# Performance work log

Hardware: AMD Instinct MI355X
Metric: run time of the kernel (lower is better)

## Reference

```python
import jax, jax.numpy as jnp
import numpy as np

D_IN, D_K, D_V = 512, 256, 256
B, S = 8, 2048

def _glorot(key, shape):
    fan_in, fan_out = shape[0], shape[-1]
    lim = np.sqrt(6.0 / (fan_in + fan_out))
    return jax.random.uniform(key, shape, jnp.float32, -lim, lim)

def setup_inputs() -> dict:
    key = jax.random.key(0)
    ks = jax.random.split(key, 9)
    return {
        "q_in": jax.random.normal(ks[0], (B, S, D_IN), jnp.float32),
        "k_in": jax.random.normal(ks[1], (B, S, D_IN), jnp.float32),
        "v_in": jax.random.normal(ks[2], (B, S, D_IN), jnp.float32),
        "Wq": _glorot(ks[3], (D_IN, D_K)),
        "bq": _glorot(ks[4], (1, D_K))[0],
        "Wk": _glorot(ks[5], (D_IN, D_K)),
        "bk": _glorot(ks[6], (1, D_K))[0],
        "Wv": _glorot(ks[7], (D_IN, D_V)),
        "bv": _glorot(ks[8], (1, D_V))[0],
    }

def reference(q_in, k_in, v_in, Wq, bq, Wk, bk, Wv, bv):
    # Dense projections (with bias, glorot-init'ed bias as in the original)
    q = q_in @ Wq + bq            # [B, S, d_k]
    k = k_in @ Wk + bk            # [B, S, d_k]
    v = v_in @ Wv + bv            # [B, S, d_v]
    scale = 1.0 / np.sqrt(D_K).astype(np.float32)
    # full attention matrix, scaled (map_fn in original == elementwise divide)
    attn = jnp.einsum('bqd,bkd->bqk', q, k) * scale  # [B, S, S]
    attn = jax.nn.softmax(attn, axis=-1)
    return jnp.einsum('bqk,bkd->bqd', attn, v)       # [B, S, d_v]
```

## Files before the change

kernel.cpp:

```cpp
#include <hip/hip_runtime.h>
#include <hip/hip_bf16.h>


typedef __attribute__((ext_vector_type(4))) float f32x4;
typedef __attribute__((ext_vector_type(8))) short s16x8;
typedef __attribute__((ext_vector_type(4))) short s16x4;

static __device__ __forceinline__ short f2bf(float x) {
  __hip_bfloat16 h = __float2bfloat16(x);
  return *reinterpret_cast<short*>(&h);
}
static __device__ __forceinline__ unsigned pack2bf(float lo, float hi) {
  return (unsigned)(unsigned short)f2bf(lo) |
         ((unsigned)(unsigned short)f2bf(hi) << 16);
}

__global__ __launch_bounds__(256) void proj3(
    const float* __restrict__ q_in, const float* __restrict__ k_in,
    const float* __restrict__ v_in, const float* __restrict__ bq,
    const float* __restrict__ bk, const float* __restrict__ bv,
    const float* __restrict__ Wq, const float* __restrict__ Wk,
    const float* __restrict__ Wv, short* __restrict__ qs,
    short* __restrict__ ks, short* __restrict__ vt) {
  const int z = blockIdx.z;
  const float* X = z == 0 ? q_in : z == 1 ? k_in : v_in;
  const float* W = z == 0 ? Wq : z == 1 ? Wk : Wv;
  const float* bias = z == 0 ? bq : z == 1 ? bk : bv;
  const float sc = z == 0 ? 0.0625f : 1.0f;
  const int n0 = blockIdx.x * 128;
  const int m0 = blockIdx.y * 128;

  __shared__ short As[128][40];
  __shared__ short Bs[128][40];

  const int tid = threadIdx.x;
  const int lane = tid & 63;
  const int wid = tid >> 6;
  const int wr = wid >> 1, wc = wid & 1;
  const int g = lane >> 4, c = lane & 15;

  f32x4 acc[4][4];
#pragma unroll
  for (int m = 0; m < 4; m++)
#pragma unroll
    for (int n = 0; n < 4; n++) acc[m][n] = (f32x4)0.0f;

  const int arow = tid >> 1, ahalf = tid & 1;
  const int bn = tid & 127, bhalf = tid >> 7;

  for (int kt = 0; kt < 16; ++kt) {
    const int k0 = kt * 32;
    const float* ap = &X[(m0 + arow) * 512 + k0 + ahalf * 16];
    f32x4 a0 = *(const f32x4*)(ap + 0);
    f32x4 a1 = *(const f32x4*)(ap + 4);
    f32x4 a2 = *(const f32x4*)(ap + 8);
    f32x4 a3 = *(const f32x4*)(ap + 12);
    float wv[16];
#pragma unroll
    for (int j = 0; j < 16; j++)
      wv[j] = W[(k0 + bhalf * 16 + j) * 256 + n0 + bn] * sc;
    __syncthreads();
    s16x8 ac0, ac1, w0, w1;
#pragma unroll
    for (int i = 0; i < 4; i++) {
      ac0[i] = f2bf(a0[i]);
      ac0[i + 4] = f2bf(a1[i]);
      ac1[i] = f2bf(a2[i]);
      ac1[i + 4] = f2bf(a3[i]);
    }
#pragma unroll
    for (int j = 0; j < 8; j++) {
      w0[j] = f2bf(wv[j]);
      w1[j] = f2bf(wv[8 + j]);
    }
    *(s16x8*)&As[arow][ahalf * 16 + 0] = ac0;
    *(s16x8*)&As[arow][ahalf * 16 + 8] = ac1;
    *(s16x8*)&Bs[bn][bhalf * 16 + 0] = w0;
    *(s16x8*)&Bs[bn][bhalf * 16 + 8] = w1;
    __syncthreads();
    s16x8 af[4], bfr[4];
#pragma unroll
    for (int m = 0; m < 4; m++)
      af[m] = *(const s16x8*)&As[wr * 64 + m * 16 + c][g * 8];
#pragma unroll
    for (int n = 0; n < 4; n++)
      bfr[n] = *(const s16x8*)&Bs[wc * 64 + n * 16 + c][g * 8];
#pragma unroll
    for (int m = 0; m < 4; m++)
#pragma unroll
      for (int n = 0; n < 4; n++)
        acc[m][n] = __builtin_amdgcn_mfma_f32_16x16x32_bf16(af[m], bfr[n],
                                                            acc[m][n], 0, 0, 0);
  }

  float bv4[4];
#pragma unroll
  for (int n = 0; n < 4; n++) bv4[n] = bias[n0 + wc * 64 + n * 16 + c] * sc;

  if (z <= 1) {
    short* outp = z == 0 ? qs : ks;
    const int ostr = z == 0 ? 512 : 256;
#pragma unroll
    for (int m = 0; m < 4; m++) {
      const int row0 = m0 + wr * 64 + m * 16 + g * 4;
#pragma unroll
      for (int n = 0; n < 4; n++) {
        const int col = n0 + wc * 64 + n * 16 + c;
#pragma unroll
        for (int r = 0; r < 4; r++)
          outp[(row0 + r) * ostr + col] = f2bf(acc[m][n][r] + bv4[n]);
      }
    }
  } else {
#pragma unroll
    for (int m = 0; m < 4; m++) {
      const int row0 = m0 + wr * 64 + m * 16 + g * 4;
      const int bb = row0 >> 11, s = row0 & 2047;
#pragma unroll
      for (int n = 0; n < 4; n++) {
        const int col = n0 + wc * 64 + n * 16 + c;
        s16x4 pk;
#pragma unroll
        for (int r = 0; r < 4; r++) pk[r] = f2bf(acc[m][n][r] + bv4[n]);
        *(s16x4*)&vt[bb * 524288 + col * 2048 + s] = pk;
      }
    }
  }
}

__global__ __launch_bounds__(512, 2) void attn_fused(
    const short* __restrict__ qs, const short* __restrict__ ks,
    const short* __restrict__ vt, float* __restrict__ out) {
  const int bid = blockIdx.x;
  const int b = bid & 7;
  const int q0 = (bid >> 3) * 64;

  __shared__ __align__(16) char smem[160256];
  short(*KsA)[264] = (short(*)[264])(smem);
  short(*VsA)[72] = (short(*)[72])(smem + 33792);
  short(*KsB)[264] = (short(*)[264])(smem + 70656);
  short(*VsB)[72] = (short(*)[72])(smem + 104448);
  short(*Ps)[16][74] = (short(*)[16][74])(smem + 141312);
  float(*Om)[260] = (float(*)[260])(smem);
  float(*Ml)[2] = (float(*)[2])(smem + 70656);

  const int tid = threadIdx.x;
  const int lane = tid & 63;
  const int wid = tid >> 6;
  const int grp = tid >> 8;
  const int gtid = tid & 255;
  const int wq = wid & 3;
  const int g = lane >> 4, c = lane & 15;

  s16x8 qf[8];
  {
    const int qrow = (b << 11) + q0 + wq * 16 + c;
#pragma unroll
    for (int d = 0; d < 8; d++)
      qf[d] = *(const s16x8*)&qs[qrow * 512 + d * 32 + g * 8];
  }

  short(*Ks)[264] = grp ? KsB : KsA;
  short(*Vs)[72] = grp ? VsB : VsA;
  const int ktbase = grp * 16;

  f32x4 o[16];
#pragma unroll
  for (int f = 0; f < 16; f++) o[f] = (f32x4)0.0f;
  float m_l = -1e30f;
  float l_l = 0.f;

  s16x8 kreg[8], vreg[8];
#pragma unroll
  for (int i = 0; i < 8; i++) {
    const int ch = gtid + i * 256;
    kreg[i] = *(const s16x8*)&ks[((b << 11) + ktbase * 64 + (ch >> 5)) * 256 +
                                 (ch & 31) * 8];
    vreg[i] = *(const s16x8*)&vt[b * 524288 + (ch >> 3) * 2048 + ktbase * 64 +
                                 (ch & 7) * 8];
  }

  for (int t = 0; t < 16; ++t) {
    __syncthreads();
#pragma unroll
    for (int i = 0; i < 8; i++) {
      const int ch = gtid + i * 256;
      *(s16x8*)&Ks[ch >> 5][(ch & 31) * 8] = kreg[i];
      *(s16x8*)&Vs[ch >> 3][(ch & 7) * 8] = vreg[i];
    }
    __syncthreads();

    if (t < 15) {
      const int kt = ktbase + t + 1;
#pragma unroll
      for (int i = 0; i < 8; i++) {
        const int ch = gtid + i * 256;
        kreg[i] = *(const s16x8*)&ks[((b << 11) + kt * 64 + (ch >> 5)) * 256 +
                                     (ch & 31) * 8];
        vreg[i] = *(const s16x8*)&vt[b * 524288 + (ch >> 3) * 2048 + kt * 64 +
                                     (ch & 7) * 8];
      }
    }

    f32x4 sf[4];
#pragma unroll
    for (int nf = 0; nf < 4; nf++) sf[nf] = (f32x4)0.0f;
    __builtin_amdgcn_s_setprio(1);
#pragma unroll
    for (int d = 0; d < 8; d++) {
#pragma unroll
      for (int nf = 0; nf < 4; nf++) {
        const s16x8 kf = *(const s16x8*)&Ks[nf * 16 + c][d * 32 + g * 8];
        sf[nf] = __builtin_amdgcn_mfma_f32_16x16x32_bf16(kf, qf[d], sf[nf], 0, 0, 0);
      }
    }
    __builtin_amdgcn_s_setprio(0);

    float mx = sf[0][0];
#pragma unroll
    for (int nf = 0; nf < 4; nf++)
#pragma unroll
      for (int r = 0; r < 4; r++) mx = fmaxf(mx, sf[nf][r]);
    mx = fmaxf(mx, __shfl_xor(mx, 16, 64));
    mx = fmaxf(mx, __shfl_xor(mx, 32, 64));
    if (__any(mx > m_l + 8.f)) {
      const float mn = fmaxf(m_l, mx);
      const float scr = __expf(m_l - mn);
      m_l = mn;
      l_l *= scr;
      float so[4];
#pragma unroll
      for (int r = 0; r < 4; r++) so[r] = __shfl(scr, g * 4 + r, 64);
#pragma unroll
      for (int f = 0; f < 16; f++)
#pragma unroll
        for (int r = 0; r < 4; r++) o[f][r] *= so[r];
    }
    float sum = 0.f;
#pragma unroll
    for (int nf = 0; nf < 4; nf++)
#pragma unroll
      for (int r = 0; r < 4; r++) {
        const float p = __expf(sf[nf][r] - m_l);
        sf[nf][r] = p;
        sum += p;
      }
    sum += __shfl_xor(sum, 16, 64);
    sum += __shfl_xor(sum, 32, 64);
    l_l += sum;

#pragma unroll
    for (int nf = 0; nf < 4; nf++)
#pragma unroll
      for (int i = 0; i < 2; i++)
        *(unsigned*)&Ps[wid][c][nf * 16 + g * 4 + 2 * i] =
            pack2bf(sf[nf][2 * i], sf[nf][2 * i + 1]);

    __builtin_amdgcn_s_setprio(1);
#pragma unroll
    for (int k2 = 0; k2 < 2; k2++) {
      const s16x8 pa = *(const s16x8*)&Ps[wid][c][k2 * 32 + g * 8];
#pragma unroll
      for (int f = 0; f < 16; f++) {
        const s16x8 vf = *(const s16x8*)&Vs[f * 16 + c][k2 * 32 + g * 8];
        o[f] = __builtin_amdgcn_mfma_f32_16x16x32_bf16(pa, vf, o[f], 0, 0, 0);
      }
    }
    __builtin_amdgcn_s_setprio(0);
  }

  float m0r[4], l0r[4];
#pragma unroll
  for (int r = 0; r < 4; r++) {
    m0r[r] = __shfl(m_l, g * 4 + r, 64);
    l0r[r] = __shfl(l_l, g * 4 + r, 64);
  }

  __syncthreads();
  if (grp == 1) {
#pragma unroll
    for (int f = 0; f < 16; f++)
#pragma unroll
      for (int r = 0; r < 4; r++)
        Om[wq * 16 + g * 4 + r][f * 16 + c] = o[f][r];
    if (g == 0) {
      Ml[wq * 16 + c][0] = m_l;
      Ml[wq * 16 + c][1] = l_l;
    }
  }
  __syncthreads();
  if (grp == 0) {
    float e0v[4], e1v[4], inv[4];
#pragma unroll
    for (int r = 0; r < 4; r++) {
      const int rw = wq * 16 + g * 4 + r;
      const float m1 = Ml[rw][0], l1 = Ml[rw][1];
      const float ms = fmaxf(m0r[r], m1);
      e0v[r] = __expf(m0r[r] - ms);
      e1v[r] = __expf(m1 - ms);
      inv[r] = 1.0f / (l0r[r] * e0v[r] + l1 * e1v[r]);
    }
#pragma unroll
    for (int f = 0; f < 16; f++) {
#pragma unroll
      for (int r = 0; r < 4; r++) {
        const int rw = wq * 16 + g * 4 + r;
        const int col = f * 16 + c;
        out[((b << 11) + q0 + rw) * 256 + col] =
            (o[f][r] * e0v[r] + Om[rw][col] * e1v[r]) * inv[r];
      }
    }
  }
}

extern "C" void kernel_launch(void* const* d_in, const int* in_sizes, int n_in,
                              void* d_out, int out_size, void* d_ws,
                              size_t ws_size, hipStream_t stream) {
  const float* q_in = (const float*)d_in[0];
  const float* k_in = (const float*)d_in[1];
  const float* v_in = (const float*)d_in[2];
  const float* Wq = (const float*)d_in[3];
  const float* bq = (const float*)d_in[4];
  const float* Wk = (const float*)d_in[5];
  const float* bk = (const float*)d_in[6];
  const float* Wv = (const float*)d_in[7];
  const float* bv = (const float*)d_in[8];
  float* out = (float*)d_out;

  char* ws = (char*)d_ws;
  short* qsb = (short*)d_out;
  short* ksb = (short*)ws;
  short* vtb = (short*)(ws + (8 << 20));

  proj3<<<dim3(2, 128, 3), dim3(256), 0, stream>>>(
      q_in, k_in, v_in, bq, bk, bv, Wq, Wk, Wv, qsb, ksb, vtb);
  attn_fused<<<dim3(256), dim3(512), 0, stream>>>(qsb, ksb, vtb, out);
}
```

Measured before the change: 120.4 us.

## Stage K/V tiles with async global_load_lds into swizzled double buffers

The projection kernel now writes K and V^T into pre-tiled 32-row blocks with an XOR swizzle. The attention kernel can then copy each tile straight into LDS using global_load_lds, double-buffered, with a single barrier per iteration. The attention block shrinks to 256 threads. Each wave now handles two 16-row query subtiles, so every K/V fragment read from LDS is reused twice, and the key tile becomes 32 wide. The aims are to remove the register round-trip staging, bank conflicts and extra barriers. The cost is more registers per wave and lower occupancy (one block per CU).

After: 141.2 us. 17.2% more time.

```diff
diff --git a/kernel.cpp b/kernel.cpp
--- a/kernel.cpp
+++ b/kernel.cpp
@@ -5,14 +5,19 @@
 typedef __attribute__((ext_vector_type(4))) float f32x4;
 typedef __attribute__((ext_vector_type(8))) short s16x8;
 typedef __attribute__((ext_vector_type(4))) short s16x4;
+typedef unsigned int u32;
 
 static __device__ __forceinline__ short f2bf(float x) {
   __hip_bfloat16 h = __float2bfloat16(x);
   return *reinterpret_cast<short*>(&h);
 }
-static __device__ __forceinline__ unsigned pack2bf(float lo, float hi) {
-  return (unsigned)(unsigned short)f2bf(lo) |
-         ((unsigned)(unsigned short)f2bf(hi) << 16);
+static __device__ __forceinline__ u32 pack2bf(float lo, float hi) {
+  return (u32)(unsigned short)f2bf(lo) | ((u32)(unsigned short)f2bf(hi) << 16);
+}
+static __device__ __forceinline__ void gload16(const void* g, void* l) {
+  __builtin_amdgcn_global_load_lds(
+      (const __attribute__((address_space(1))) u32*)g,
+      (__attribute__((address_space(3))) u32*)l, 16, 0, 0);
 }
 
 __global__ __launch_bounds__(256) void proj3(
@@ -21,7 +26,7 @@
     const float* __restrict__ bk, const float* __restrict__ bv,
     const float* __restrict__ Wq, const float* __restrict__ Wk,
     const float* __restrict__ Wv, short* __restrict__ qs,
-    short* __restrict__ ks, short* __restrict__ vt) {
+    char* __restrict__ ks, char* __restrict__ vt) {
   const int z = blockIdx.z;
   const float* X = z == 0 ? q_in : z == 1 ? k_in : v_in;
   const float* W = z == 0 ? Wq : z == 1 ? Wk : Wv;
@@ -97,9 +102,7 @@
 #pragma unroll
   for (int n = 0; n < 4; n++) bv4[n] = bias[n0 + wc * 64 + n * 16 + c] * sc;
 
-  if (z <= 1) {
-    short* outp = z == 0 ? qs : ks;
-    const int ostr = z == 0 ? 512 : 256;
+  if (z == 0) {
 #pragma unroll
     for (int m = 0; m < 4; m++) {
       const int row0 = m0 + wr * 64 + m * 16 + g * 4;
@@ -108,7 +111,25 @@
         const int col = n0 + wc * 64 + n * 16 + c;
 #pragma unroll
         for (int r = 0; r < 4; r++)
-          outp[(row0 + r) * ostr + col] = f2bf(acc[m][n][r] + bv4[n]);
+          qs[(row0 + r) * 512 + col] = f2bf(acc[m][n][r] + bv4[n]);
+      }
+    }
+  } else if (z == 1) {
+#pragma unroll
+    for (int m = 0; m < 4; m++) {
+      const int row0 = m0 + wr * 64 + m * 16 + g * 4;
+#pragma unroll
+      for (int n = 0; n < 4; n++) {
+        const int col = n0 + wc * 64 + n * 16 + c;
+#pragma unroll
+        for (int r = 0; r < 4; r++) {
+          const int rowg = row0 + r;
+          const int bb = rowg >> 11, s = rowg & 2047;
+          const int tt = s >> 5, rr = s & 31;
+          const u32 off = (u32)(rr * 512 + col * 2) ^ ((u32)(rr & 7) << 4);
+          *(short*)(ks + ((size_t)(bb * 64 + tt) << 14) + off) =
+              f2bf(acc[m][n][r] + bv4[n]);
+        }
       }
     }
   } else {
@@ -116,198 +137,216 @@
     for (int m = 0; m < 4; m++) {
       const int row0 = m0 + wr * 64 + m * 16 + g * 4;
       const int bb = row0 >> 11, s = row0 & 2047;
+      const int tt = s >> 5, kvl = s & 31;
 #pragma unroll
       for (int n = 0; n < 4; n++) {
         const int col = n0 + wc * 64 + n * 16 + c;
         s16x4 pk;
 #pragma unroll
         for (int r = 0; r < 4; r++) pk[r] = f2bf(acc[m][n][r] + bv4[n]);
-        *(s16x4*)&vt[bb * 524288 + col * 2048 + s] = pk;
-      }
-    }
-  }
-}
-
-__global__ __launch_bounds__(512, 2) void attn_fused(
-    const short* __restrict__ qs, const short* __restrict__ ks,
-    const short* __restrict__ vt, float* __restrict__ out) {
+        const u32 off = (u32)(col * 64 + kvl * 2) ^ ((u32)(col & 7) << 4);
+        *(s16x4*)(vt + ((size_t)(bb * 64 + tt) << 14) + off) = pk;
+      }
+    }
+  }
+}
+
+__global__ __launch_bounds__(256, 1) void attn_fused(
+    const short* __restrict__ qs, const char* __restrict__ ksb,
+    const char* __restrict__ vtb, float* __restrict__ out) {
   const int bid = blockIdx.x;
   const int b = bid & 7;
   const int q0 = (bid >> 3) * 64;
 
-  __shared__ __align__(16) char smem[160256];
-  short(*KsA)[264] = (short(*)[264])(smem);
-  short(*VsA)[72] = (short(*)[72])(smem + 33792);
-  short(*KsB)[264] = (short(*)[264])(smem + 70656);
-  short(*VsB)[72] = (short(*)[72])(smem + 104448);
-  short(*Ps)[16][74] = (short(*)[16][74])(smem + 141312);
-  float(*Om)[260] = (float(*)[260])(smem);
-  float(*Ml)[2] = (float(*)[2])(smem + 70656);
+  __shared__ __align__(16) char smem[141312];
 
   const int tid = threadIdx.x;
   const int lane = tid & 63;
   const int wid = tid >> 6;
-  const int grp = tid >> 8;
-  const int gtid = tid & 255;
-  const int wq = wid & 3;
+  const int grp = wid >> 1;
+  const int wq = wid & 1;
   const int g = lane >> 4, c = lane & 15;
 
-  s16x8 qf[8];
-  {
-    const int qrow = (b << 11) + q0 + wq * 16 + c;
+  const char* ktiles = ksb + ((size_t)b << 20);
+  const char* vtiles = vtb + ((size_t)b << 20);
+
+  char* kbase[2] = {smem + grp * 65536, smem + grp * 65536 + 32768};
+  char* vbase[2] = {kbase[0] + 16384, kbase[1] + 16384};
+  short* Ps = (short*)(smem + 131072 + wid * 2560);
+
+  s16x8 qf[2][8];
+#pragma unroll
+  for (int qsub = 0; qsub < 2; qsub++) {
+    const int qrow = (b << 11) + q0 + wq * 32 + qsub * 16 + c;
 #pragma unroll
     for (int d = 0; d < 8; d++)
-      qf[d] = *(const s16x8*)&qs[qrow * 512 + d * 32 + g * 8];
-  }
-
-  short(*Ks)[264] = grp ? KsB : KsA;
-  short(*Vs)[72] = grp ? VsB : VsA;
-  const int ktbase = grp * 16;
-
-  f32x4 o[16];
-#pragma unroll
-  for (int f = 0; f < 16; f++) o[f] = (f32x4)0.0f;
-  float m_l = -1e30f;
-  float l_l = 0.f;
-
-  s16x8 kreg[8], vreg[8];
-#pragma unroll
-  for (int i = 0; i < 8; i++) {
-    const int ch = gtid + i * 256;
-    kreg[i] = *(const s16x8*)&ks[((b << 11) + ktbase * 64 + (ch >> 5)) * 256 +
-                                 (ch & 31) * 8];
-    vreg[i] = *(const s16x8*)&vt[b * 524288 + (ch >> 3) * 2048 + ktbase * 64 +
-                                 (ch & 7) * 8];
-  }
-
-  for (int t = 0; t < 16; ++t) {
+      qf[qsub][d] = *(const s16x8*)&qs[qrow * 512 + d * 32 + g * 8];
+  }
+
+  f32x4 o[2][16];
+#pragma unroll
+  for (int qsub = 0; qsub < 2; qsub++)
+#pragma unroll
+    for (int f = 0; f < 16; f++) o[qsub][f] = (f32x4)0.0f;
+  float m_l[2] = {-1e30f, -1e30f};
+  float l_l[2] = {0.f, 0.f};
+
+  const u32 xr = (u32)(c & 7) << 4;
+
+  auto STAGE = [&](int t, int sel) {
+    const char* src = (wq == 0 ? ktiles : vtiles) +
+                      ((size_t)(grp * 32 + t) << 14) + lane * 16;
+    char* dst = wq == 0 ? kbase[sel] : vbase[sel];
+#pragma unroll
+    for (int i = 0; i < 16; i++) gload16(src + i * 1024, dst + i * 1024);
+  };
+
+  STAGE(0, 0);
+  __syncthreads();
+
+  for (int t = 0; t < 32; ++t) {
+    const int sel = t & 1;
+    if (t < 31) STAGE(t + 1, sel ^ 1);
+
+    const char* Kb = kbase[sel];
+    const char* Vb = vbase[sel];
+
+    f32x4 sf[2][2];
+#pragma unroll
+    for (int qsub = 0; qsub < 2; qsub++)
+#pragma unroll
+      for (int nf = 0; nf < 2; nf++) sf[qsub][nf] = (f32x4)0.0f;
+    __builtin_amdgcn_s_setprio(1);
+#pragma unroll
+    for (int d = 0; d < 8; ++d) {
+      const u32 k0off = ((u32)(c * 512 + d * 64 + g * 16)) ^ xr;
+      const s16x8 kf0 = *(const s16x8*)(Kb + k0off);
+      const s16x8 kf1 = *(const s16x8*)(Kb + (k0off + 8192));
+#pragma unroll
+      for (int qsub = 0; qsub < 2; qsub++) {
+        sf[qsub][0] = __builtin_amdgcn_mfma_f32_16x16x32_bf16(kf0, qf[qsub][d],
+                                                              sf[qsub][0], 0, 0, 0);
+        sf[qsub][1] = __builtin_amdgcn_mfma_f32_16x16x32_bf16(kf1, qf[qsub][d],
+                                                              sf[qsub][1], 0, 0, 0);
+      }
+    }
+    __builtin_amdgcn_s_setprio(0);
+
+    float mx[2];
+#pragma unroll
+    for (int qsub = 0; qsub < 2; qsub++) {
+      float m0 = sf[qsub][0][0];
+#pragma unroll
+      for (int nf = 0; nf < 2; nf++)
+#pragma unroll
+        for (int r = 0; r < 4; r++) m0 = fmaxf(m0, sf[qsub][nf][r]);
+      m0 = fmaxf(m0, __shfl_xor(m0, 16, 64));
+      m0 = fmaxf(m0, __shfl_xor(m0, 32, 64));
+      mx[qsub] = m0;
+    }
+    if (__any((mx[0] > m_l[0] + 8.f) | (mx[1] > m_l[1] + 8.f))) {
+#pragma unroll
+      for (int qsub = 0; qsub < 2; qsub++) {
+        const float mn = fmaxf(m_l[qsub], mx[qsub]);
+        const float scr = __expf(m_l[qsub] - mn);
+        m_l[qsub] = mn;
+        l_l[qsub] *= scr;
+        float so[4];
+#pragma unroll
+        for (int r = 0; r < 4; r++) so[r] = __shfl(scr, g * 4 + r, 64);
+#pragma unroll
+        for (int f = 0; f < 16; f++)
+#pragma unroll
+          for (int r = 0; r < 4; r++) o[qsub][f][r] *= so[r];
+      }
+    }
+#pragma unroll
+    for (int qsub = 0; qsub < 2; qsub++) {
+      float sum = 0.f;
+#pragma unroll
+      for (int nf = 0; nf < 2; nf++)
+#pragma unroll
+        for (int r = 0; r < 4; r++) {
+          const float p = __expf(sf[qsub][nf][r] - m_l[qsub]);
+          sf[qsub][nf][r] = p;
+          sum += p;
+        }
+      sum += __shfl_xor(sum, 16, 64);
+      sum += __shfl_xor(sum, 32, 64);
+      l_l[qsub] += sum;
+    }
+
+#pragma unroll
+    for (int qsub = 0; qsub < 2; qsub++)
+#pragma unroll
+      for (int nf = 0; nf < 2; nf++) {
+        const int base = (qsub * 16 + c) * 40 + nf * 16 + g * 4;
+        *(u32*)&Ps[base] = pack2bf(sf[qsub][nf][0], sf[qsub][nf][1]);
+        *(u32*)&Ps[base + 2] = pack2bf(sf[qsub][nf][2], sf[qsub][nf][3]);
+      }
+
+    s16x8 pa[2];
+    pa[0] = *(const s16x8*)&Ps[c * 40 + g * 8];
+    pa[1] = *(const s16x8*)&Ps[(16 + c) * 40 + g * 8];
+    __builtin_amdgcn_s_setprio(1);
+#pragma unroll
+    for (int f = 0; f < 16; ++f) {
+      const u32 voff = ((u32)((f * 16 + c) * 64 + g * 16)) ^ xr;
+      const s16x8 vf = *(const s16x8*)(Vb + voff);
+      o[0][f] = __builtin_amdgcn_mfma_f32_16x16x32_bf16(pa[0], vf, o[0][f], 0, 0, 0);
+      o[1][f] = __builtin_amdgcn_mfma_f32_16x16x32_bf16(pa[1], vf, o[1][f], 0, 0, 0);
+    }
+    __builtin_amdgcn_s_setprio(0);
+
     __syncthreads();
-#pragma unroll
-    for (int i = 0; i < 8; i++) {
-      const int ch = gtid + i * 256;
-      *(s16x8*)&Ks[ch >> 5][(ch & 31) * 8] = kreg[i];
-      *(s16x8*)&Vs[ch >> 3][(ch & 7) * 8] = vreg[i];
-    }
-    __syncthreads();
-
-    if (t < 15) {
-      const int kt = ktbase + t + 1;
-#pragma unroll
-      for (int i = 0; i < 8; i++) {
-        const int ch = gtid + i * 256;
-        kreg[i] = *(const s16x8*)&ks[((b << 11) + kt * 64 + (ch >> 5)) * 256 +
-                                     (ch & 31) * 8];
-        vreg[i] = *(const s16x8*)&vt[b * 524288 + (ch >> 3) * 2048 + kt * 64 +
-                                     (ch & 7) * 8];
-      }
-    }
-
-    f32x4 sf[4];
-#pragma unroll
-    for (int nf = 0; nf < 4; nf++) sf[nf] = (f32x4)0.0f;
-    __builtin_amdgcn_s_setprio(1);
-#pragma unroll
-    for (int d = 0; d < 8; d++) {
-#pragma unroll
-      for (int nf = 0; nf < 4; nf++) {
-        const s16x8 kf = *(const s16x8*)&Ks[nf * 16 + c][d * 32 + g * 8];
-        sf[nf] = __builtin_amdgcn_mfma_f32_16x16x32_bf16(kf, qf[d], sf[nf], 0, 0, 0);
-      }
-    }
-    __builtin_amdgcn_s_setprio(0);
-
-    float mx = sf[0][0];
-#pragma unroll
-    for (int nf = 0; nf < 4; nf++)
-#pragma unroll
-      for (int r = 0; r < 4; r++) mx = fmaxf(mx, sf[nf][r]);
-    mx = fmaxf(mx, __shfl_xor(mx, 16, 64));
-    mx = fmaxf(mx, __shfl_xor(mx, 32, 64));
-    if (__any(mx > m_l + 8.f)) {
-      const float mn = fmaxf(m_l, mx);
-      const float scr = __expf(m_l - mn);
-      m_l = mn;
-      l_l *= scr;
-      float so[4];
-#pragma unroll
-      for (int r = 0; r < 4; r++) so[r] = __shfl(scr, g * 4 + r, 64);
+  }
+
+  float(*Om)[260] = (float(*)[260])smem;
+  float(*Ml)[2] = (float(*)[2])(smem + 66560);
+  float m0r[2][4], l0r[2][4];
+#pragma unroll
+  for (int qsub = 0; qsub < 2; qsub++)
+#pragma unroll
+    for (int r = 0; r < 4; r++) {
+      m0r[qsub][r] = __shfl(m_l[qsub], g * 4 + r, 64);
+      l0r[qsub][r] = __shfl(l_l[qsub], g * 4 + r, 64);
+    }
+  if (grp == 1) {
+#pragma unroll
+    for (int qsub = 0; qsub < 2; qsub++) {
 #pragma unroll
       for (int f = 0; f < 16; f++)
 #pragma unroll
-        for (int r = 0; r < 4; r++) o[f][r] *= so[r];
-    }
-    float sum = 0.f;
-#pragma unroll
-    for (int nf = 0; nf < 4; nf++)
-#pragma unroll
-      for (int r = 0; r < 4; r++) {
-        const float p = __expf(sf[nf][r] - m_l);
-        sf[nf][r] = p;
-        sum += p;
-      }
-    sum += __shfl_xor(sum, 16, 64);
-    sum += __shfl_xor(sum, 32, 64);
-    l_l += sum;
-
-#pragma unroll
-    for (int nf = 0; nf < 4; nf++)
-#pragma unroll
-      for (int i = 0; i < 2; i++)
-        *(unsigned*)&Ps[wid][c][nf * 16 + g * 4 + 2 * i] =
-            pack2bf(sf[nf][2 * i], sf[nf][2 * i + 1]);
-
-    __builtin_amdgcn_s_setprio(1);
-#pragma unroll
-    for (int k2 = 0; k2 < 2; k2++) {
-      const s16x8 pa = *(const s16x8*)&Ps[wid][c][k2 * 32 + g * 8];
-#pragma unroll
-      for (int f = 0; f < 16; f++) {
-        const s16x8 vf = *(const s16x8*)&Vs[f * 16 + c][k2 * 32 + g * 8];
-        o[f] = __builtin_amdgcn_mfma_f32_16x16x32_bf16(pa, vf, o[f], 0, 0, 0);
-      }
-    }
-    __builtin_amdgcn_s_setprio(0);
-  }
-
-  float m0r[4], l0r[4];
-#pragma unroll
-  for (int r = 0; r < 4; r++) {
-    m0r[r] = __shfl(m_l, g * 4 + r, 64);
-    l0r[r] = __shfl(l_l, g * 4 + r, 64);
-  }
-
-  __syncthreads();
-  if (grp == 1) {
-#pragma unroll
-    for (int f = 0; f < 16; f++)
-#pragma unroll
-      for (int r = 0; r < 4; r++)
-        Om[wq * 16 + g * 4 + r][f * 16 + c] = o[f][r];
-    if (g == 0) {
-      Ml[wq * 16 + c][0] = m_l;
-      Ml[wq * 16 + c][1] = l_l;
+        for (int r = 0; r < 4; r++)
+          Om[wq * 32 + qsub * 16 + g * 4 + r][f * 16 + c] = o[qsub][f][r];
+      if (g == 0) {
+        Ml[wq * 32 + qsub * 16 + c][0] = m_l[qsub];
+        Ml[wq * 32 + qsub * 16 + c][1] = l_l[qsub];
+      }
     }
   }
   __syncthreads();
   if (grp == 0) {
-    float e0v[4], e1v[4], inv[4];
-#pragma unroll
-    for (int r = 0; r < 4; r++) {
-      const int rw = wq * 16 + g * 4 + r;
-      const float m1 = Ml[rw][0], l1 = Ml[rw][1];
-      const float ms = fmaxf(m0r[r], m1);
-      e0v[r] = __expf(m0r[r] - ms);
-      e1v[r] = __expf(m1 - ms);
-      inv[r] = 1.0f / (l0r[r] * e0v[r] + l1 * e1v[r]);
-    }
-#pragma unroll
-    for (int f = 0; f < 16; f++) {
+#pragma unroll
+    for (int qsub = 0; qsub < 2; qsub++) {
+      float e0v[4], e1v[4], inv[4];
 #pragma unroll
       for (int r = 0; r < 4; r++) {
-        const int rw = wq * 16 + g * 4 + r;
-        const int col = f * 16 + c;
-        out[((b << 11) + q0 + rw) * 256 + col] =
-            (o[f][r] * e0v[r] + Om[rw][col] * e1v[r]) * inv[r];
+        const int rw = wq * 32 + qsub * 16 + g * 4 + r;
+        const float m1 = Ml[rw][0], l1 = Ml[rw][1];
+        const float ms = fmaxf(m0r[qsub][r], m1);
+        e0v[r] = __expf(m0r[qsub][r] - ms);
+        e1v[r] = __expf(m1 - ms);
+        inv[r] = 1.0f / (l0r[qsub][r] * e0v[r] + l1 * e1v[r]);
+      }
+#pragma unroll
+      for (int f = 0; f < 16; f++) {
+#pragma unroll
+        for (int r = 0; r < 4; r++) {
+          const int rw = wq * 32 + qsub * 16 + g * 4 + r;
+          out[((b << 11) + q0 + rw) * 256 + f * 16 + c] =
+              (o[qsub][f][r] * e0v[r] + Om[rw][f * 16 + c] * e1v[r]) * inv[r];
+        }
       }
     }
   }
@@ -329,10 +368,10 @@
 
   char* ws = (char*)d_ws;
   short* qsb = (short*)d_out;
-  short* ksb = (short*)ws;
-  short* vtb = (short*)(ws + (8 << 20));
+  char* ksb = ws;
+  char* vtb = ws + (8 << 20);
 
   proj3<<<dim3(2, 128, 3), dim3(256), 0, stream>>>(
       q_in, k_in, v_in, bq, bk, bv, Wq, Wk, Wv, qsb, ksb, vtb);
-  attn_fused<<<dim3(256), dim3(512), 0, stream>>>(qsb, ksb, vtb, out);
-}
+  attn_fused<<<dim3(256), dim3(256), 0, stream>>>(qsb, ksb, vtb, out);
+}
```

## Pre-tile and swizzle K/V in projection, stage via direct global-to-LDS loads

Applied to the files above, without the earlier changes.

The projection kernel now writes K and V^T into per-32-key tiles with an XOR swizzle, so the attention kernel can copy each tile straight into LDS with global_load_lds. This replaces the register-staged copy and its extra barrier. The attention loop now uses 32-key tiles with double buffering, a smaller Ps buffer, and launch bounds of one block per CU. The projection grid is also flattened and remapped to reorder blocks across XCDs. The risks are lower occupancy, twice as many loop iterations each with a barrier, and scattered 2-byte stores for K in the projection.

Result: faster. 105.0 us (-12.8%).

```diff
diff --git a/kernel.cpp b/kernel.cpp
--- a/kernel.cpp
+++ b/kernel.cpp
@@ -5,14 +5,19 @@
 typedef __attribute__((ext_vector_type(4))) float f32x4;
 typedef __attribute__((ext_vector_type(8))) short s16x8;
 typedef __attribute__((ext_vector_type(4))) short s16x4;
+typedef unsigned int u32;
 
 static __device__ __forceinline__ short f2bf(float x) {
   __hip_bfloat16 h = __float2bfloat16(x);
   return *reinterpret_cast<short*>(&h);
 }
-static __device__ __forceinline__ unsigned pack2bf(float lo, float hi) {
-  return (unsigned)(unsigned short)f2bf(lo) |
-         ((unsigned)(unsigned short)f2bf(hi) << 16);
+static __device__ __forceinline__ u32 pack2bf(float lo, float hi) {
+  return (u32)(unsigned short)f2bf(lo) | ((u32)(unsigned short)f2bf(hi) << 16);
+}
+static __device__ __forceinline__ void gload16(const void* g, void* l) {
+  __builtin_amdgcn_global_load_lds(
+      (const __attribute__((address_space(1))) u32*)g,
+      (__attribute__((address_space(3))) u32*)l, 16, 0, 0);
 }
 
 __global__ __launch_bounds__(256) void proj3(
@@ -21,14 +26,17 @@
     const float* __restrict__ bk, const float* __restrict__ bv,
     const float* __restrict__ Wq, const float* __restrict__ Wk,
     const float* __restrict__ Wv, short* __restrict__ qs,
-    short* __restrict__ ks, short* __restrict__ vt) {
-  const int z = blockIdx.z;
+    char* __restrict__ ks, char* __restrict__ vt) {
+  const int flat = blockIdx.x;
+  const int ord = (flat & 7) * 96 + (flat >> 3);
+  const int z = ord >> 8;
+  const int rem = ord & 255;
+  const int n0 = (rem & 1) * 128;
+  const int m0 = (rem >> 1) * 128;
   const float* X = z == 0 ? q_in : z == 1 ? k_in : v_in;
   const float* W = z == 0 ? Wq : z == 1 ? Wk : Wv;
   const float* bias = z == 0 ? bq : z == 1 ? bk : bv;
   const float sc = z == 0 ? 0.0625f : 1.0f;
-  const int n0 = blockIdx.x * 128;
-  const int m0 = blockIdx.y * 128;
 
   __shared__ short As[128][40];
   __shared__ short Bs[128][40];
@@ -97,9 +105,7 @@
 #pragma unroll
   for (int n = 0; n < 4; n++) bv4[n] = bias[n0 + wc * 64 + n * 16 + c] * sc;
 
-  if (z <= 1) {
-    short* outp = z == 0 ? qs : ks;
-    const int ostr = z == 0 ? 512 : 256;
+  if (z == 0) {
 #pragma unroll
     for (int m = 0; m < 4; m++) {
       const int row0 = m0 + wr * 64 + m * 16 + g * 4;
@@ -108,7 +114,25 @@
         const int col = n0 + wc * 64 + n * 16 + c;
 #pragma unroll
         for (int r = 0; r < 4; r++)
-          outp[(row0 + r) * ostr + col] = f2bf(acc[m][n][r] + bv4[n]);
+          qs[(row0 + r) * 512 + col] = f2bf(acc[m][n][r] + bv4[n]);
+      }
+    }
+  } else if (z == 1) {
+#pragma unroll
+    for (int m = 0; m < 4; m++) {
+      const int row0 = m0 + wr * 64 + m * 16 + g * 4;
+#pragma unroll
+      for (int n = 0; n < 4; n++) {
+        const int col = n0 + wc * 64 + n * 16 + c;
+#pragma unroll
+        for (int r = 0; r < 4; r++) {
+          const int rowg = row0 + r;
+          const int bb = rowg >> 11, s = rowg & 2047;
+          const int tt = s >> 5, rr = s & 31;
+          const u32 off = (u32)(rr * 512 + col * 2) ^ ((u32)(rr & 7) << 4);
+          *(short*)(ks + ((size_t)(bb * 64 + tt) << 14) + off) =
+              f2bf(acc[m][n][r] + bv4[n]);
+        }
       }
     }
   } else {
@@ -116,41 +140,42 @@
     for (int m = 0; m < 4; m++) {
       const int row0 = m0 + wr * 64 + m * 16 + g * 4;
       const int bb = row0 >> 11, s = row0 & 2047;
+      const int tt = s >> 5, kvl = s & 31;
 #pragma unroll
       for (int n = 0; n < 4; n++) {
         const int col = n0 + wc * 64 + n * 16 + c;
         s16x4 pk;
 #pragma unroll
         for (int r = 0; r < 4; r++) pk[r] = f2bf(acc[m][n][r] + bv4[n]);
-        *(s16x4*)&vt[bb * 524288 + col * 2048 + s] = pk;
-      }
-    }
-  }
-}
-
-__global__ __launch_bounds__(512, 2) void attn_fused(
-    const short* __restrict__ qs, const short* __restrict__ ks,
-    const short* __restrict__ vt, float* __restrict__ out) {
+        const u32 off = (u32)(col * 64 + kvl * 2) ^ ((u32)(col & 7) << 4);
+        *(s16x4*)(vt + ((size_t)(bb * 64 + tt) << 14) + off) = pk;
+      }
+    }
+  }
+}
+
+__global__ __launch_bounds__(512, 1) void attn_fused(
+    const short* __restrict__ qs, const char* __restrict__ ksb,
+    const char* __restrict__ vtb, float* __restrict__ out) {
   const int bid = blockIdx.x;
   const int b = bid & 7;
   const int q0 = (bid >> 3) * 64;
 
-  __shared__ __align__(16) char smem[160256];
-  short(*KsA)[264] = (short(*)[264])(smem);
-  short(*VsA)[72] = (short(*)[72])(smem + 33792);
-  short(*KsB)[264] = (short(*)[264])(smem + 70656);
-  short(*VsB)[72] = (short(*)[72])(smem + 104448);
-  short(*Ps)[16][74] = (short(*)[16][74])(smem + 141312);
-  float(*Om)[260] = (float(*)[260])(smem);
-  float(*Ml)[2] = (float(*)[2])(smem + 70656);
+  __shared__ __align__(16) char smem[141312];
 
   const int tid = threadIdx.x;
   const int lane = tid & 63;
   const int wid = tid >> 6;
-  const int grp = tid >> 8;
+  const int grp = wid >> 2;
+  const int wq = wid & 3;
   const int gtid = tid & 255;
-  const int wq = wid & 3;
   const int g = lane >> 4, c = lane & 15;
+
+  const char* ktiles = ksb + ((size_t)b << 20);
+  const char* vtiles = vtb + ((size_t)b << 20);
+
+  char* gbase = smem + grp * 65536;
+  short* Ps = (short*)(smem + 131072 + wid * 1280);
 
   s16x8 qf[8];
   {
@@ -160,65 +185,54 @@
       qf[d] = *(const s16x8*)&qs[qrow * 512 + d * 32 + g * 8];
   }
 
-  short(*Ks)[264] = grp ? KsB : KsA;
-  short(*Vs)[72] = grp ? VsB : VsA;
-  const int ktbase = grp * 16;
-
   f32x4 o[16];
 #pragma unroll
   for (int f = 0; f < 16; f++) o[f] = (f32x4)0.0f;
   float m_l = -1e30f;
   float l_l = 0.f;
 
-  s16x8 kreg[8], vreg[8];
-#pragma unroll
-  for (int i = 0; i < 8; i++) {
-    const int ch = gtid + i * 256;
-    kreg[i] = *(const s16x8*)&ks[((b << 11) + ktbase * 64 + (ch >> 5)) * 256 +
-                                 (ch & 31) * 8];
-    vreg[i] = *(const s16x8*)&vt[b * 524288 + (ch >> 3) * 2048 + ktbase * 64 +
-                                 (ch & 7) * 8];
-  }
-
-  for (int t = 0; t < 16; ++t) {
-    __syncthreads();
-#pragma unroll
-    for (int i = 0; i < 8; i++) {
-      const int ch = gtid + i * 256;
-      *(s16x8*)&Ks[ch >> 5][(ch & 31) * 8] = kreg[i];
-      *(s16x8*)&Vs[ch >> 3][(ch & 7) * 8] = vreg[i];
-    }
-    __syncthreads();
-
-    if (t < 15) {
-      const int kt = ktbase + t + 1;
-#pragma unroll
-      for (int i = 0; i < 8; i++) {
-        const int ch = gtid + i * 256;
-        kreg[i] = *(const s16x8*)&ks[((b << 11) + kt * 64 + (ch >> 5)) * 256 +
-                                     (ch & 31) * 8];
-        vreg[i] = *(const s16x8*)&vt[b * 524288 + (ch >> 3) * 2048 + kt * 64 +
-                                     (ch & 7) * 8];
-      }
-    }
-
-    f32x4 sf[4];
-#pragma unroll
-    for (int nf = 0; nf < 4; nf++) sf[nf] = (f32x4)0.0f;
+  const u32 xr = (u32)(c & 7) << 4;
+
+  auto STAGE = [&](int t, int sel) {
+    const size_t toff = (size_t)(grp * 32 + t) << 14;
+    char* kd = gbase + sel * 32768;
+    char* vd = kd + 16384;
+    const char* ksrc = ktiles + toff + gtid * 16;
+    const char* vsrc = vtiles + toff + gtid * 16;
+#pragma unroll
+    for (int i = 0; i < 4; i++) {
+      gload16(ksrc + i * 4096, kd + gtid * 16 + i * 4096);
+      gload16(vsrc + i * 4096, vd + gtid * 16 + i * 4096);
+    }
+  };
+
+  STAGE(0, 0);
+  __syncthreads();
+
+  for (int t = 0; t < 32; ++t) {
+    const int sel = t & 1;
+    if (t < 31) STAGE(t + 1, sel ^ 1);
+
+    const char* Kb = gbase + sel * 32768;
+    const char* Vb = Kb + 16384;
+
+    f32x4 sf[2];
+    sf[0] = (f32x4)0.0f;
+    sf[1] = (f32x4)0.0f;
     __builtin_amdgcn_s_setprio(1);
 #pragma unroll
-    for (int d = 0; d < 8; d++) {
-#pragma unroll
-      for (int nf = 0; nf < 4; nf++) {
-        const s16x8 kf = *(const s16x8*)&Ks[nf * 16 + c][d * 32 + g * 8];
-        sf[nf] = __builtin_amdgcn_mfma_f32_16x16x32_bf16(kf, qf[d], sf[nf], 0, 0, 0);
-      }
+    for (int d = 0; d < 8; ++d) {
+      const u32 k0off = ((u32)(c * 512 + d * 64 + g * 16)) ^ xr;
+      const s16x8 kf0 = *(const s16x8*)(Kb + k0off);
+      const s16x8 kf1 = *(const s16x8*)(Kb + (k0off + 8192));
+      sf[0] = __builtin_amdgcn_mfma_f32_16x16x32_bf16(kf0, qf[d], sf[0], 0, 0, 0);
+      sf[1] = __builtin_amdgcn_mfma_f32_16x16x32_bf16(kf1, qf[d], sf[1], 0, 0, 0);
     }
     __builtin_amdgcn_s_setprio(0);
 
     float mx = sf[0][0];
 #pragma unroll
-    for (int nf = 0; nf < 4; nf++)
+    for (int nf = 0; nf < 2; nf++)
 #pragma unroll
       for (int r = 0; r < 4; r++) mx = fmaxf(mx, sf[nf][r]);
     mx = fmaxf(mx, __shfl_xor(mx, 16, 64));
@@ -238,7 +252,7 @@
     }
     float sum = 0.f;
 #pragma unroll
-    for (int nf = 0; nf < 4; nf++)
+    for (int nf = 0; nf < 2; nf++)
 #pragma unroll
       for (int r = 0; r < 4; r++) {
         const float p = __expf(sf[nf][r] - m_l);
@@ -250,33 +264,33 @@
     l_l += sum;
 
 #pragma unroll
-    for (int nf = 0; nf < 4; nf++)
-#pragma unroll
-      for (int i = 0; i < 2; i++)
-        *(unsigned*)&Ps[wid][c][nf * 16 + g * 4 + 2 * i] =
-            pack2bf(sf[nf][2 * i], sf[nf][2 * i + 1]);
-
+    for (int nf = 0; nf < 2; nf++) {
+      const int base = c * 40 + nf * 16 + g * 4;
+      *(u32*)&Ps[base] = pack2bf(sf[nf][0], sf[nf][1]);
+      *(u32*)&Ps[base + 2] = pack2bf(sf[nf][2], sf[nf][3]);
+    }
+
+    const s16x8 pa = *(const s16x8*)&Ps[c * 40 + g * 8];
     __builtin_amdgcn_s_setprio(1);
 #pragma unroll
-    for (int k2 = 0; k2 < 2; k2++) {
-      const s16x8 pa = *(const s16x8*)&Ps[wid][c][k2 * 32 + g * 8];
-#pragma unroll
-      for (int f = 0; f < 16; f++) {
-        const s16x8 vf = *(const s16x8*)&Vs[f * 16 + c][k2 * 32 + g * 8];
-        o[f] = __builtin_amdgcn_mfma_f32_16x16x32_bf16(pa, vf, o[f], 0, 0, 0);
-      }
+    for (int f = 0; f < 16; ++f) {
+      const u32 voff = ((u32)((f * 16 + c) * 64 + g * 16)) ^ xr;
+      const s16x8 vf = *(const s16x8*)(Vb + voff);
+      o[f] = __builtin_amdgcn_mfma_f32_16x16x32_bf16(pa, vf, o[f], 0, 0, 0);
     }
     __builtin_amdgcn_s_setprio(0);
-  }
-
+
+    __syncthreads();
+  }
+
+  float(*Om)[260] = (float(*)[260])smem;
+  float(*Ml)[2] = (float(*)[2])(smem + 66560);
   float m0r[4], l0r[4];
 #pragma unroll
   for (int r = 0; r < 4; r++) {
     m0r[r] = __shfl(m_l, g * 4 + r, 64);
     l0r[r] = __shfl(l_l, g * 4 + r, 64);
   }
-
-  __syncthreads();
   if (grp == 1) {
 #pragma unroll
     for (int f = 0; f < 16; f++)
@@ -305,9 +319,8 @@
 #pragma unroll
       for (int r = 0; r < 4; r++) {
         const int rw = wq * 16 + g * 4 + r;
-        const int col = f * 16 + c;
-        out[((b << 11) + q0 + rw) * 256 + col] =
-            (o[f][r] * e0v[r] + Om[rw][col] * e1v[r]) * inv[r];
+        out[((b << 11) + q0 + rw) * 256 + f * 16 + c] =
+            (o[f][r] * e0v[r] + Om[rw][f * 16 + c] * e1v[r]) * inv[r];
       }
     }
   }
@@ -329,10 +342,10 @@
 
   char* ws = (char*)d_ws;
   short* qsb = (short*)d_out;
-  short* ksb = (short*)ws;
-  short* vtb = (short*)(ws + (8 << 20));
-
-  proj3<<<dim3(2, 128, 3), dim3(256), 0, stream>>>(
-      q_in, k_in, v_in, bq, bk, bv, Wq, Wk, Wv, qsb, ksb, vtb);
+  char* ksb = ws;
+  char* vtb = ws + (8 << 20);
+
+  proj3<<<dim3(768), dim3(256), 0, stream>>>(q_in, k_in, v_in, bq, bk, bv, Wq,
+                                             Wk, Wv, qsb, ksb, vtb);
   attn_fused<<<dim3(256), dim3(512), 0, stream>>>(qsb, ksb, vtb, out);
 }
```
